# Kernel tuning notes

Measured on AMD Instinct MI355X. Metric: run time of the kernel, lower is better.

Reference implementation:

```python
import jax, jax.numpy as jnp
import numpy as np

IN_CH = 256
NUM_CLASSES = 1
CONF_THR = 0.3
NMS_IOU = 0.2
ANCHOR_SIZES = (32.0, 64.0, 128.0)
ASPECTS = (0.5, 1.0, 2.0)
NUM_ANCHORS = len(ANCHOR_SIZES) * len(ASPECTS)  # 9
K_CAND = 1024   # top-score candidates fed to NMS per image
MAX_DET = 100   # max_output_size in source
BN_EPS = 1e-5


def _anchors():
    a = [[s * r / 224.0, s / r / 224.0] for s in ANCHOR_SIZES for r in ASPECTS]
    return jnp.asarray(a, jnp.float32)  # [A, 2] (w, h)


def _conv(x, w, b, pad):
    y = jax.lax.conv_general_dilated(x, w, (1, 1), [(pad, pad), (pad, pad)],
                                     dimension_numbers=('NCHW', 'OIHW', 'NCHW'))
    return y + b[None, :, None, None]


def _bn(x, g, b, m, v):
    inv = jax.lax.rsqrt(v + BN_EPS)
    return (x - m[None, :, None, None]) * (g * inv)[None, :, None, None] + b[None, :, None, None]


def _corners(b):
    return (b[..., 0] - b[..., 2] / 2, b[..., 1] - b[..., 3] / 2,
            b[..., 0] + b[..., 2] / 2, b[..., 1] + b[..., 3] / 2)


def _iou_one(box, boxes):
    # box: [4] cxcywh, boxes: [K,4] -> iou [K]
    ax1, ay1, ax2, ay2 = _corners(box)
    bx1, by1, bx2, by2 = _corners(boxes)
    iw = jnp.maximum(jnp.minimum(ax2, bx2) - jnp.maximum(ax1, bx1), 0.0)
    ih = jnp.maximum(jnp.minimum(ay2, by2) - jnp.maximum(ay1, by1), 0.0)
    inter = iw * ih
    union = (ax2 - ax1) * (ay2 - ay1) + (bx2 - bx1) * (by2 - by1) - inter
    return inter / (union + 1e-16)


def _nms(boxes, scores):
    # boxes [K,4], scores [K] -> kept boxes padded to [MAX_DET,4]
    s0 = jnp.where(scores > CONF_THR, scores, -1.0)

    def body(i, carry):
        s, out = carry
        j = jnp.argmax(s)
        ok = s[j] > 0.0
        box = boxes[j]
        iou = _iou_one(box, boxes)
        s_new = jnp.where(iou > NMS_IOU, -1.0, s).at[j].set(-1.0)
        s = jnp.where(ok, s_new, s)
        out = out.at[i].set(jnp.where(ok, box, jnp.zeros_like(box)))
        return s, out

    _, out = jax.lax.fori_loop(0, MAX_DET, body,
                               (s0, jnp.zeros((MAX_DET, 4), boxes.dtype)))
    return out


def _forward(features, w1, b1, g1, be1, m1, v1, w2, b2, g2, be2, m2, v2, wo, bo):
    x = jax.nn.relu(_bn(_conv(features, w1, b1, 1), g1, be1, m1, v1))
    x = jax.nn.relu(_bn(_conv(x, w2, b2, 1), g2, be2, m2, v2))
    p = _conv(x, wo, bo, 0)                      # [B, A*(5+C), H, W]
    B, _, H, W = p.shape
    p = p.reshape(B, NUM_ANCHORS, 5 + NUM_CLASSES, H, W).transpose(0, 3, 4, 1, 2)  # [B,H,W,A,5+C]
    obj = jax.nn.sigmoid(p[..., 4])
    anch = _anchors()
    gx = jnp.arange(W, dtype=p.dtype)[None, :, None]
    gy = jnp.arange(H, dtype=p.dtype)[:, None, None]
    px = (jax.nn.sigmoid(p[..., 0]) + gx) / W
    py = (jax.nn.sigmoid(p[..., 1]) + gy) / H
    pw = jnp.exp(p[..., 2]) * anch[:, 0]
    ph = jnp.exp(p[..., 3]) * anch[:, 1]
    boxes = jnp.stack([px, py, pw, ph], -1).reshape(B, -1, 4)
    if NUM_CLASSES > 1:
        scores = obj * jax.nn.sigmoid(p[..., 5:]).max(-1)
    else:
        scores = obj
    scores = scores.reshape(B, -1)

    def per_image(bx, sc):
        top_s, idx = jax.lax.top_k(sc, K_CAND)
        return _nms(bx[idx], top_s)

    return jax.vmap(per_image)(boxes, scores)    # [B, MAX_DET, 4]


def setup_inputs() -> dict:
    key = jax.random.key(0)
    ks = jax.random.split(key, 16)
    B = 32
    c1, c2 = IN_CH // 2, IN_CH // 4
    oc = NUM_ANCHORS * (5 + NUM_CLASSES)
    return {
        'features': jax.random.normal(ks[0], (B, IN_CH, 56, 56), jnp.float32),
        'w1': jax.random.normal(ks[1], (c1, IN_CH, 3, 3), jnp.float32) * 0.02,
        'b1': jax.random.normal(ks[2], (c1,), jnp.float32) * 0.02,
        'g1': 1.0 + 0.1 * jax.random.normal(ks[3], (c1,), jnp.float32),
        'be1': 0.1 * jax.random.normal(ks[4], (c1,), jnp.float32),
        'm1': 0.1 * jax.random.normal(ks[5], (c1,), jnp.float32),
        'v1': jax.random.uniform(ks[6], (c1,), jnp.float32, 0.5, 1.5),
        'w2': jax.random.normal(ks[7], (c2, c1, 3, 3), jnp.float32) * 0.03,
        'b2': jax.random.normal(ks[8], (c2,), jnp.float32) * 0.02,
        'g2': 1.0 + 0.1 * jax.random.normal(ks[9], (c2,), jnp.float32),
        'be2': 0.1 * jax.random.normal(ks[10], (c2,), jnp.float32),
        'm2': 0.1 * jax.random.normal(ks[11], (c2,), jnp.float32),
        'v2': jax.random.uniform(ks[12], (c2,), jnp.float32, 0.5, 1.5),
        'wo': jax.random.normal(ks[13], (oc, c2, 1, 1), jnp.float32) * 0.1,
        'bo': jax.random.normal(ks[14], (oc,), jnp.float32) * 0.05,
    }


def reference(features, w1, b1, g1, be1, m1, v1, w2, b2, g2, be2, m2, v2, wo, bo):
    return _forward(features, w1, b1, g1, be1, m1, v1, w2, b2, g2, be2, m2, v2, wo, bo)
```

## Files before the change

### kernel.cpp

```cpp
#include <hip/hip_runtime.h>
#include <math.h>
#include <stdint.h>

constexpr int BB   = 32;
constexpr int HW   = 3136;
constexpr int C0   = 256, C1 = 128, C2 = 64;
constexpr int NA   = 9;
constexpr int NCAND = HW * NA;
constexpr int KSEL  = 1024;
constexpr int MAXDET = 100;

typedef _Float16 half8 __attribute__((ext_vector_type(8)));
typedef _Float16 half4v __attribute__((ext_vector_type(4)));
typedef float    f32x4  __attribute__((ext_vector_type(4)));
typedef float    f32x16 __attribute__((ext_vector_type(16)));

__device__ __forceinline__ void g2l16(const void* g, void* l) {
    auto gp = reinterpret_cast<const __attribute__((address_space(1))) char*>(
        reinterpret_cast<uintptr_t>(g));
    auto lp = reinterpret_cast<__attribute__((address_space(3))) char*>(
        reinterpret_cast<uintptr_t>(l));
    __builtin_amdgcn_global_load_lds(gp, lp, 16, 0, 0);
}

__global__ void bn_prep2(const float* g1, const float* be1, const float* m1,
                         const float* v1, const float* cb1,
                         const float* g2, const float* be2, const float* m2,
                         const float* v2, const float* cb2,
                         float* scl1, float* tb1, float* scl2, float* tb2) {
    int i = threadIdx.x;
    if (i < C1) {
        float inv = 1.f / sqrtf(v1[i] + 1e-5f);
        float s = g1[i] * inv;
        scl1[i] = s;
        tb1[i] = be1[i] + (cb1[i] - m1[i]) * s;
    }
    if (i < C2) {
        float inv = 1.f / sqrtf(v2[i] + 1e-5f);
        float s = g2[i] * inv;
        scl2[i] = s;
        tb2[i] = be2[i] + (cb2[i] - m2[i]) * s;
    }
}

__device__ __forceinline__ void reorder_one(const float* w, _Float16* wc,
                                            int i, int CIN, int COUT) {
    int K = CIN * 9;
    int ci  = i & 31;
    int row = (i >> 5) % (2 * COUT);
    int ch  = (i >> 5) / (2 * COUT);
    int pl  = row / COUT;
    int oc  = row - pl * COUT;
    int cg = ch / 9, r = ch - cg * 9;
    int cin = cg * 32 + ci;
    float v = w[oc * K + cin * 9 + r];
    _Float16 h = (_Float16)v;
    wc[i] = pl ? (_Float16)(v - (float)h) : h;
}

__global__ void reorder_w_both(const float* __restrict__ w1, _Float16* __restrict__ w1c,
                               const float* __restrict__ w2, _Float16* __restrict__ w2c) {
    constexpr int N1 = 2 * C1 * C0 * 9;
    constexpr int N2 = 2 * C2 * C1 * 9;
    int i = blockIdx.x * 256 + threadIdx.x;
    if (i < N1) reorder_one(w1, w1c, i, C0, C1);
    else if (i < N1 + N2) reorder_one(w2, w2c, i - N1, C1, C2);
}

__global__ __launch_bounds__(256) void nchw_to_nhwc_split(
    const float* __restrict__ in, _Float16* __restrict__ hi, _Float16* __restrict__ lo)
{
    __shared__ float tile[64 * 68];
    const int pt = blockIdx.x * 64, ct = blockIdx.y * 64, b = blockIdx.z;
    const int t = threadIdx.x;
    const int r0 = t >> 4, cidx = (t & 15) * 4;
#pragma unroll
    for (int rr = 0; rr < 64; rr += 16) {
        int r = rr + r0;
        const float* src = in + ((size_t)(b * 256 + ct + r)) * HW + pt + cidx;
        float4 v = *(const float4*)src;
        float* d = &tile[r * 68 + cidx];
        d[0] = v.x; d[1] = v.y; d[2] = v.z; d[3] = v.w;
    }
    __syncthreads();
    const int p = t >> 2, c0 = (t & 3) * 16;
    size_t obase = ((size_t)(b * HW + pt + p)) * 256 + ct + c0;
    half8 h0, h1, l0, l1;
#pragma unroll
    for (int j = 0; j < 16; ++j) {
        float v = tile[(c0 + j) * 68 + p];
        _Float16 hh = (_Float16)v;
        _Float16 ll = (_Float16)(v - (float)hh);
        if (j < 8) { h0[j] = hh; l0[j] = ll; }
        else       { h1[j - 8] = hh; l1[j - 8] = ll; }
    }
    *(half8*)(hi + obase)     = h0;
    *(half8*)(hi + obase + 8) = h1;
    *(half8*)(lo + obase)     = l0;
    *(half8*)(lo + obase + 8) = l1;
}

template <int CIN, int COUT, int MINW, bool NHWC_OUT>
__global__ __launch_bounds__(256, MINW) void conv3x3_v12(
    const _Float16* __restrict__ xhi,
    const _Float16* __restrict__ xlo,
    const _Float16* __restrict__ wc,
    const _Float16* __restrict__ zbuf,
    const float* __restrict__ scl, const float* __restrict__ tb,
    _Float16* __restrict__ ohi,
    _Float16* __restrict__ olo,
    float* __restrict__ onchw)
{
    constexpr int K       = CIN * 9;
    constexpr int NCH     = K / 32;
    constexpr int WROWS   = 2 * COUT;
    constexpr int CHALVES = WROWS * 32;
    constexpr int WI      = WROWS / 64;
    constexpr int PI      = 2;
    constexpr int WOC     = COUT / 64;

    __shared__ __align__(16) _Float16 SP[128 * 64];
    __shared__ __align__(16) _Float16 SW[WROWS * 32];

    const int bid = blockIdx.x;
    const int swz = (bid & 7) * (gridDim.x >> 3) + (bid >> 3);
    const int b = swz / 25;
    const int pixBase = (swz - b * 25) * 128;
    const int bHW = b * HW;

    const int t = threadIdx.x, l = t & 63, w = t >> 6;

    const int cpix = (l & 7) ^ ((l >> 3) & 7);
    const int ppl = cpix >> 2, pq = cpix & 3;
    const _Float16* xsp = ppl ? xlo : xhi;
    int py[4], px[4];
    const _Float16* pbase[4];
#pragma unroll
    for (int i = 0; i < 4; ++i) {
        int p = w * 32 + i * 8 + (l >> 3);
        int pix = pixBase + p;
        py[i] = pix / 56; px[i] = pix - py[i] * 56;
        pbase[i] = xsp + (size_t)(bHW + pix) * CIN + pq * 8;
    }
    const _Float16* wbase = wc + ((size_t)(w * (WI * 16) + (l >> 2))) * 32 + (l & 3) * 8;

    const int wid = t >> 6;
    const int wp = wid & 1, wo = wid >> 1;
    const int lc = l & 31, lk = l >> 5;

    f32x16 acc[PI][WOC];
#pragma unroll
    for (int pi = 0; pi < PI; ++pi)
#pragma unroll
        for (int oi = 0; oi < WOC; ++oi) acc[pi][oi] = (f32x16)0.f;

    auto stage = [&](int ch) {
        int cg = ch / 9, r = ch - cg * 9;
        int ky = r / 3;
        int dy = ky - 1, dx = (r - ky * 3) - 1;
        int off = (dy * 56 + dx) * CIN + cg * 32;
#pragma unroll
        for (int i = 0; i < 4; ++i) {
            bool v = ((unsigned)(py[i] + dy) < 56u) && ((unsigned)(px[i] + dx) < 56u);
            const void* src = v ? (const void*)(pbase[i] + off) : (const void*)zbuf;
            g2l16(src, (void*)&SP[w * 2048 + i * 512]);
        }
        const _Float16* wsrc = wbase + (size_t)ch * CHALVES;
#pragma unroll
        for (int j = 0; j < WI; ++j)
            g2l16((const void*)(wsrc + j * 512), (void*)&SW[(w * WI + j) * 512]);
    };

    auto compute = [&]() {
#pragma unroll
        for (int ks = 0; ks < 2; ++ks) {
            half8 pb[PI][2];
#pragma unroll
            for (int pi = 0; pi < PI; ++pi) {
                int prw = wp * (PI * 32) + pi * 32 + lc;
                int key = prw & 7;
#pragma unroll
                for (int pl2 = 0; pl2 < 2; ++pl2) {
                    int c = pl2 * 4 + ks * 2 + lk;
                    pb[pi][pl2] = *(const half8*)&SP[prw * 64 + ((c ^ key) << 3)];
                }
            }
            half8 wa[WOC][2];
#pragma unroll
            for (int oi = 0; oi < WOC; ++oi)
#pragma unroll
                for (int pl2 = 0; pl2 < 2; ++pl2) {
                    int row = pl2 * COUT + wo * (WOC * 32) + oi * 32 + lc;
                    int c = ks * 2 + lk;
                    wa[oi][pl2] = *(const half8*)&SW[row * 32 + (c << 3)];
                }
#pragma unroll
            for (int pi = 0; pi < PI; ++pi)
#pragma unroll
                for (int oi = 0; oi < WOC; ++oi) {
                    acc[pi][oi] = __builtin_amdgcn_mfma_f32_32x32x16_f16(wa[oi][0], pb[pi][0], acc[pi][oi], 0, 0, 0);
                    acc[pi][oi] = __builtin_amdgcn_mfma_f32_32x32x16_f16(wa[oi][0], pb[pi][1], acc[pi][oi], 0, 0, 0);
                    acc[pi][oi] = __builtin_amdgcn_mfma_f32_32x32x16_f16(wa[oi][1], pb[pi][0], acc[pi][oi], 0, 0, 0);
                }
        }
    };

    for (int ch = 0; ch < NCH; ++ch) {
        stage(ch);
        __syncthreads();
        compute();
        __syncthreads();
    }

#pragma unroll
    for (int pi = 0; pi < PI; ++pi) {
        const int pix = pixBase + wp * (PI * 32) + pi * 32 + lc;
        if (pix < HW) {
#pragma unroll
            for (int oi = 0; oi < WOC; ++oi) {
#pragma unroll
                for (int g = 0; g < 4; ++g) {
                    const int oc0 = wo * (WOC * 32) + oi * 32 + 8 * g + 4 * lk;
                    f32x4 s4 = *(const f32x4*)(scl + oc0);
                    f32x4 t4 = *(const f32x4*)(tb + oc0);
                    if constexpr (NHWC_OUT) {
                        half4v hh, ll;
#pragma unroll
                        for (int m2 = 0; m2 < 4; ++m2) {
                            float val = fmaxf(acc[pi][oi][g * 4 + m2] * s4[m2] + t4[m2], 0.f);
                            _Float16 h = (_Float16)val;
                            hh[m2] = h;
                            ll[m2] = (_Float16)(val - (float)h);
                        }
                        size_t o = ((size_t)(bHW + pix)) * COUT + oc0;
                        *(half4v*)(ohi + o) = hh;
                        *(half4v*)(olo + o) = ll;
                    } else {
#pragma unroll
                        for (int m2 = 0; m2 < 4; ++m2) {
                            float val = fmaxf(acc[pi][oi][g * 4 + m2] * s4[m2] + t4[m2], 0.f);
                            onchw[((size_t)(b * COUT + oc0 + m2)) * HW + pix] = val;
                        }
                    }
                }
            }
        }
    }
}

__global__ __launch_bounds__(256) void conv1x1_decode(
    const float* __restrict__ x2, const float* __restrict__ wo,
    const float* __restrict__ bo,
    float* __restrict__ boxes, float* __restrict__ scores)
{
    __shared__ float ws[64 * 56];
    for (int i = threadIdx.x; i < 54 * 64; i += 256) {
        int oc = i % 54, c = i / 54;
        ws[c * 56 + oc] = wo[oc * 64 + c];
    }
    __syncthreads();

    int u = blockIdx.x * 256 + threadIdx.x;
    int a = u % 9;
    int rest = u / 9;
    int quad = rest % 784;
    int b = rest / 784;
    int pix0 = quad * 4;
    int y = pix0 / 56;
    int x0 = pix0 - y * 56;

    const float* xb = x2 + (size_t)b * 64 * HW + pix0;
    float acc[5][4];
#pragma unroll
    for (int j = 0; j < 5; ++j)
#pragma unroll
        for (int p = 0; p < 4; ++p) acc[j][p] = 0.f;

#pragma unroll 8
    for (int c = 0; c < 64; ++c) {
        float4 xv = *(const float4*)(xb + c * HW);
#pragma unroll
        for (int j = 0; j < 5; ++j) {
            float w = ws[c * 56 + a * 6 + j];
            acc[j][0] += w * xv.x;
            acc[j][1] += w * xv.y;
            acc[j][2] += w * xv.z;
            acc[j][3] += w * xv.w;
        }
    }

    int si = a / 3, ri = a - si * 3;
    float sv = (float)(32 << si);
    float rv = 0.5f * (float)(1 << ri);
    float aw = (sv * rv) / 224.f;
    float ah = (sv / rv) / 224.f;
    float bo0 = bo[a * 6 + 0], bo1 = bo[a * 6 + 1], bo2 = bo[a * 6 + 2];
    float bo3 = bo[a * 6 + 3], bo4 = bo[a * 6 + 4];

#pragma unroll
    for (int p = 0; p < 4; ++p) {
        float p0 = acc[0][p] + bo0;
        float p1 = acc[1][p] + bo1;
        float p2 = acc[2][p] + bo2;
        float p3 = acc[3][p] + bo3;
        float p4 = acc[4][p] + bo4;
        float sx = 1.f / (1.f + expf(-p0));
        float sy = 1.f / (1.f + expf(-p1));
        float pxc = (sx + (float)(x0 + p)) / 56.f;
        float pyc = (sy + (float)y) / 56.f;
        float pw = expf(p2) * aw;
        float ph = expf(p3) * ah;
        float sc = 1.f / (1.f + expf(-p4));
        int n = (y * 56 + x0 + p) * 9 + a;
        float4 bx; bx.x = pxc; bx.y = pyc; bx.z = pw; bx.w = ph;
        *(float4*)&boxes[((size_t)b * NCAND + n) * 4] = bx;
        scores[(size_t)b * NCAND + n] = sc;
    }
}

__device__ __forceinline__ unsigned fkey(float f) {
    unsigned u = __float_as_uint(f);
    return (u & 0x80000000u) ? ~u : (u | 0x80000000u);
}

__global__ __launch_bounds__(1024) void topk_select(
    const float* __restrict__ scores, const float* __restrict__ boxes,
    float* __restrict__ cbox, float* __restrict__ csc, int* __restrict__ cidx)
{
    const int b = blockIdx.x, t = threadIdx.x;
    const float* sp = scores + (size_t)b * NCAND;
    const int lane = t & 63, w = t >> 6;

    __shared__ unsigned hist[2048];
    __shared__ unsigned gsum[64];
    __shared__ unsigned wsum[16];
    __shared__ unsigned s_sel, s_need, s_tot0, s_tot1;

    unsigned prefix = 0x80000000u, maskSo = 0x80000000u;
    int need = KSEL;

    for (int round = 0; round < 3; ++round) {
        const int shift = (round == 0) ? 20 : (round == 1 ? 10 : 0);
        const unsigned bmask = (round == 0) ? 2047u : 1023u;
        const int ngroups = (round == 0) ? 64 : 32;

        hist[t] = 0;
        if (round == 0) hist[t + 1024] = 0;
        __syncthreads();
        for (int i = t; i < NCAND; i += 1024) {
            unsigned u = fkey(sp[i]);
            if ((u & maskSo) == prefix) atomicAdd(&hist[(u >> shift) & bmask], 1u);
        }
        __syncthreads();
        if (t < ngroups) {
            unsigned s = 0;
#pragma unroll 8
            for (int k = 0; k < 32; ++k) s += hist[t * 32 + k];
            gsum[t] = s;
        }
        __syncthreads();
        if (t == 0) {
            int rem = need;
            int g = ngroups - 1;
            for (;; --g) {
                if ((int)gsum[g] >= rem || g == 0) break;
                rem -= (int)gsum[g];
            }
            unsigned sel = (unsigned)(g * 32);
            for (int v = g * 32 + 31; v >= g * 32; --v) {
                int c = (int)hist[v];
                if (c >= rem || v == g * 32) { sel = (unsigned)v; break; }
                rem -= c;
            }
            s_sel = sel; s_need = (unsigned)rem;
        }
        __syncthreads();
        prefix |= (s_sel << shift);
        maskSo |= (bmask << shift);
        need = (int)s_need;
        __syncthreads();
    }

    const unsigned cutoff = prefix;
    const unsigned needT = (unsigned)need;
    unsigned outBase = 0, tieBase = 0;
    const unsigned long long mlt = (1ull << lane) - 1ull;

    for (int c0 = 0; c0 < NCAND; c0 += 1024) {
        int i = c0 + t;
        bool valid = i < NCAND;
        float sc = valid ? sp[i] : 0.f;
        unsigned u = valid ? fkey(sc) : 0u;
        bool gt = valid && (u > cutoff);
        bool eq = valid && (u == cutoff);

        unsigned long long balE = __ballot(eq);
        unsigned lpE = (unsigned)__popcll(balE & mlt);
        if (lane == 0) wsum[w] = (unsigned)__popcll(balE);
        __syncthreads();
        if (t == 0) {
            unsigned run = 0;
            for (int k = 0; k < 16; ++k) { unsigned x = wsum[k]; wsum[k] = run; run += x; }
            s_tot1 = run;
        }
        __syncthreads();
        unsigned tieRank = tieBase + wsum[w] + lpE;
        bool take = gt || (eq && tieRank < needT);
        __syncthreads();

        unsigned long long balT = __ballot(take);
        unsigned lpT = (unsigned)__popcll(balT & mlt);
        if (lane == 0) wsum[w] = (unsigned)__popcll(balT);
        __syncthreads();
        if (t == 0) {
            unsigned run = 0;
            for (int k = 0; k < 16; ++k) { unsigned x = wsum[k]; wsum[k] = run; run += x; }
            s_tot0 = run;
        }
        __syncthreads();
        unsigned pos = outBase + wsum[w] + lpT;
        if (take) {
            float4 bx = *(const float4*)&boxes[((size_t)b * NCAND + i) * 4];
            *(float4*)&cbox[((size_t)b * KSEL + pos) * 4] = bx;
            csc[(size_t)b * KSEL + pos] = sc;
            cidx[(size_t)b * KSEL + pos] = i;
        }
        tieBase += s_tot1;
        outBase += s_tot0;
        __syncthreads();
    }
}

__global__ __launch_bounds__(64) void nms_wave(
    const float* __restrict__ cbox, const float* __restrict__ csc,
    const int* __restrict__ cidx, float* __restrict__ out)
{
    const int b = blockIdx.x, l = threadIdx.x;
    float cx[16], cy[16], w_[16], h_[16], s[16];
    int id[16];
#pragma unroll
    for (int j = 0; j < 16; ++j) {
        int ci = (b << 10) + (j << 6) + l;
        float4 bb = *(const float4*)&cbox[(size_t)ci * 4];
        float sc = csc[ci];
        cx[j] = bb.x; cy[j] = bb.y; w_[j] = bb.z; h_[j] = bb.w;
        s[j] = sc > 0.3f ? sc : -1.f;
        id[j] = cidx[ci];
    }
    float* ob = out + (size_t)b * MAXDET * 4;

    for (int it = 0; it < MAXDET; ++it) {
        float bs = s[0]; int bi = id[0];
        float bcx = cx[0], bcy = cy[0], bw = w_[0], bh = h_[0];
#pragma unroll
        for (int j = 1; j < 16; ++j) {
            bool tk = (s[j] > bs) || (s[j] == bs && id[j] < bi);
            if (tk) { bs = s[j]; bi = id[j]; bcx = cx[j]; bcy = cy[j]; bw = w_[j]; bh = h_[j]; }
        }
#pragma unroll
        for (int m2 = 1; m2 < 64; m2 <<= 1) {
            float os = __shfl_xor(bs, m2); int oi = __shfl_xor(bi, m2);
            float ox = __shfl_xor(bcx, m2), oy = __shfl_xor(bcy, m2);
            float ow = __shfl_xor(bw, m2), oh2 = __shfl_xor(bh, m2);
            bool tk = (os > bs) || (os == bs && oi < bi);
            if (tk) { bs = os; bi = oi; bcx = ox; bcy = oy; bw = ow; bh = oh2; }
        }
        if (bs <= 0.f) {
            for (int q = it * 4 + l; q < MAXDET * 4; q += 64) ob[q] = 0.f;
            break;
        }
        if (l == 0) {
            float4 o; o.x = bcx; o.y = bcy; o.z = bw; o.w = bh;
            *(float4*)&ob[it * 4] = o;
        }
        float wx1 = bcx - bw / 2.f, wy1 = bcy - bh / 2.f;
        float wx2 = bcx + bw / 2.f, wy2 = bcy + bh / 2.f;
        float war = (wx2 - wx1) * (wy2 - wy1);
#pragma unroll
        for (int j = 0; j < 16; ++j) {
            float jx1 = cx[j] - w_[j] / 2.f, jy1 = cy[j] - h_[j] / 2.f;
            float jx2 = cx[j] + w_[j] / 2.f, jy2 = cy[j] + h_[j] / 2.f;
            float iw = fminf(wx2, jx2) - fmaxf(wx1, jx1); iw = fmaxf(iw, 0.f);
            float ih = fminf(wy2, jy2) - fmaxf(wy1, jy1); ih = fmaxf(ih, 0.f);
            float inter = iw * ih;
            float jar = (jx2 - jx1) * (jy2 - jy1);
            float uni = war + jar - inter;
            if (inter / (uni + 1e-16f) > 0.2f) s[j] = -1.f;
        }
    }
}

extern "C" void kernel_launch(void* const* d_in, const int* in_sizes, int n_in,
                              void* d_out, int out_size, void* d_ws, size_t ws_size,
                              hipStream_t stream)
{
    const float* features = (const float*)d_in[0];
    const float* w1 = (const float*)d_in[1];
    const float* b1 = (const float*)d_in[2];
    const float* g1 = (const float*)d_in[3];
    const float* be1 = (const float*)d_in[4];
    const float* m1 = (const float*)d_in[5];
    const float* v1 = (const float*)d_in[6];
    const float* w2 = (const float*)d_in[7];
    const float* b2 = (const float*)d_in[8];
    const float* g2 = (const float*)d_in[9];
    const float* be2 = (const float*)d_in[10];
    const float* m2 = (const float*)d_in[11];
    const float* v2 = (const float*)d_in[12];
    const float* wo = (const float*)d_in[13];
    const float* bo = (const float*)d_in[14];

    char* ws = (char*)d_ws;
    size_t off = 0;
    auto alloc = [&](size_t bytes) {
        char* p = ws + off;
        off += (bytes + 255) / 256 * 256;
        return p;
    };

    _Float16* zbuf = (_Float16*)alloc(256);
    _Float16* w1c = (_Float16*)alloc((size_t)2 * C1 * 2304 * 2);
    _Float16* w2c = (_Float16*)alloc((size_t)2 * C2 * 1152 * 2);
    float* scl1 = (float*)alloc(C1 * 4);
    float* tb1  = (float*)alloc(C1 * 4);
    float* scl2 = (float*)alloc(C2 * 4);
    float* tb2  = (float*)alloc(C2 * 4);

    const size_t planeF = (size_t)BB * HW * C0 * 2;
    char* regB = alloc(2 * planeF);
    _Float16* fhi = (_Float16*)regB;
    _Float16* flo = (_Float16*)(regB + planeF);

    const size_t planeX1 = (size_t)BB * HW * C1 * 2;
    char* regC = alloc(2 * planeX1);
    _Float16* x1hi = (_Float16*)regC;
    _Float16* x1lo = (_Float16*)(regC + planeX1);

    float* x2     = (float*)regB;
    float* boxes  = (float*)(regB + 25690112);
    float* scores = (float*)(regB + 25690112 + 14450688);
    float* cbox = (float*)regC;
    float* csc  = (float*)(regC + 524288);
    int*   cidx = (int*)(regC + 524288 + 131072);

    hipMemsetAsync(zbuf, 0, 256, stream);
    bn_prep2<<<1, 256, 0, stream>>>(g1, be1, m1, v1, b1, g2, be2, m2, v2, b2,
                                    scl1, tb1, scl2, tb2);
    {
        int total = 2 * C1 * 2304 + 2 * C2 * 1152;
        reorder_w_both<<<(total + 255) / 256, 256, 0, stream>>>(w1, w1c, w2, w2c);
    }

    nchw_to_nhwc_split<<<dim3(49, 4, BB), 256, 0, stream>>>(features, fhi, flo);

    conv3x3_v12<C0, C1, 4, true><<<800, 256, 0, stream>>>(
        fhi, flo, w1c, zbuf, scl1, tb1, x1hi, x1lo, nullptr);
    conv3x3_v12<C1, C2, 4, false><<<800, 256, 0, stream>>>(
        x1hi, x1lo, w2c, zbuf, scl2, tb2, nullptr, nullptr, x2);

    conv1x1_decode<<<(BB * 784 * NA) / 256, 256, 0, stream>>>(x2, wo, bo, boxes, scores);

    topk_select<<<BB, 1024, 0, stream>>>(scores, boxes, cbox, csc, cidx);
    nms_wave<<<BB, 64, 0, stream>>>(cbox, csc, cidx, (float*)d_out);
}
```

Baseline: 608.9 us.

## Fuse 1x1 head conv and box decode into second 3x3 conv epilogue

The second 3x3 conv no longer writes the fp32 NCHW x2 tensor to global memory. Its epilogue stores the BN+ReLU outputs for its 128-pixel tile into shared memory, loads the 1x1 head weights, and runs the head conv plus sigmoid/exp box decode in place, writing boxes and scores directly. This removes a full kernel launch and the global write and reread of x2. In exchange it adds a larger LDS arena, lowers the min-waves launch bound to 3, and runs a serial per-thread 64-wide dot-product tail after the MFMA loop.

```diff
diff --git a/kernel.cpp b/kernel.cpp
--- a/kernel.cpp
+++ b/kernel.cpp
@@ -100,8 +100,8 @@
     *(half8*)(lo + obase + 8) = l1;
 }
 
-template <int CIN, int COUT, int MINW, bool NHWC_OUT>
-__global__ __launch_bounds__(256, MINW) void conv3x3_v12(
+template <int CIN, int COUT, int MINW, bool DEC>
+__global__ __launch_bounds__(256, MINW) void conv3x3_v15(
     const _Float16* __restrict__ xhi,
     const _Float16* __restrict__ xlo,
     const _Float16* __restrict__ wc,
@@ -109,7 +109,10 @@
     const float* __restrict__ scl, const float* __restrict__ tb,
     _Float16* __restrict__ ohi,
     _Float16* __restrict__ olo,
-    float* __restrict__ onchw)
+    const float* __restrict__ wox,
+    const float* __restrict__ box,
+    float* __restrict__ boxes,
+    float* __restrict__ scores)
 {
     constexpr int K       = CIN * 9;
     constexpr int NCH     = K / 32;
@@ -119,8 +122,12 @@
     constexpr int PI      = 2;
     constexpr int WOC     = COUT / 64;
 
-    __shared__ __align__(16) _Float16 SP[128 * 64];
-    __shared__ __align__(16) _Float16 SW[WROWS * 32];
+    constexpr size_t ARENA = DEC ? (33280 + 14336) : (16384 + (size_t)WROWS * 64);
+    __shared__ __align__(16) char arena[ARENA];
+    _Float16* SP = (_Float16*)arena;
+    _Float16* SW = (_Float16*)(arena + 16384);
+    float* x2t = (float*)arena;
+    float* wsd = (float*)(arena + 33280);
 
     const int bid = blockIdx.x;
     const int swz = (bid & 7) * (gridDim.x >> 3) + (bid >> 3);
@@ -212,18 +219,18 @@
         __syncthreads();
     }
 
-#pragma unroll
-    for (int pi = 0; pi < PI; ++pi) {
-        const int pix = pixBase + wp * (PI * 32) + pi * 32 + lc;
-        if (pix < HW) {
-#pragma unroll
-            for (int oi = 0; oi < WOC; ++oi) {
-#pragma unroll
-                for (int g = 0; g < 4; ++g) {
-                    const int oc0 = wo * (WOC * 32) + oi * 32 + 8 * g + 4 * lk;
-                    f32x4 s4 = *(const f32x4*)(scl + oc0);
-                    f32x4 t4 = *(const f32x4*)(tb + oc0);
-                    if constexpr (NHWC_OUT) {
+    if constexpr (!DEC) {
+#pragma unroll
+        for (int pi = 0; pi < PI; ++pi) {
+            const int pix = pixBase + wp * (PI * 32) + pi * 32 + lc;
+            if (pix < HW) {
+#pragma unroll
+                for (int oi = 0; oi < WOC; ++oi) {
+#pragma unroll
+                    for (int g = 0; g < 4; ++g) {
+                        const int oc0 = wo * (WOC * 32) + oi * 32 + 8 * g + 4 * lk;
+                        f32x4 s4 = *(const f32x4*)(scl + oc0);
+                        f32x4 t4 = *(const f32x4*)(tb + oc0);
                         half4v hh, ll;
 #pragma unroll
                         for (int m2 = 0; m2 < 4; ++m2) {
@@ -235,86 +242,73 @@
                         size_t o = ((size_t)(bHW + pix)) * COUT + oc0;
                         *(half4v*)(ohi + o) = hh;
                         *(half4v*)(olo + o) = ll;
-                    } else {
-#pragma unroll
-                        for (int m2 = 0; m2 < 4; ++m2) {
-                            float val = fmaxf(acc[pi][oi][g * 4 + m2] * s4[m2] + t4[m2], 0.f);
-                            onchw[((size_t)(b * COUT + oc0 + m2)) * HW + pix] = val;
-                        }
                     }
                 }
             }
         }
-    }
-}
-
-__global__ __launch_bounds__(256) void conv1x1_decode(
-    const float* __restrict__ x2, const float* __restrict__ wo,
-    const float* __restrict__ bo,
-    float* __restrict__ boxes, float* __restrict__ scores)
-{
-    __shared__ float ws[64 * 56];
-    for (int i = threadIdx.x; i < 54 * 64; i += 256) {
-        int oc = i % 54, c = i / 54;
-        ws[c * 56 + oc] = wo[oc * 64 + c];
-    }
-    __syncthreads();
-
-    int u = blockIdx.x * 256 + threadIdx.x;
-    int a = u % 9;
-    int rest = u / 9;
-    int quad = rest % 784;
-    int b = rest / 784;
-    int pix0 = quad * 4;
-    int y = pix0 / 56;
-    int x0 = pix0 - y * 56;
-
-    const float* xb = x2 + (size_t)b * 64 * HW + pix0;
-    float acc[5][4];
-#pragma unroll
-    for (int j = 0; j < 5; ++j)
-#pragma unroll
-        for (int p = 0; p < 4; ++p) acc[j][p] = 0.f;
-
+    } else {
+#pragma unroll
+        for (int pi = 0; pi < PI; ++pi) {
+            const int lp = wp * (PI * 32) + pi * 32 + lc;
+#pragma unroll
+            for (int g = 0; g < 4; ++g) {
+                const int oc0 = wo * 32 + 8 * g + 4 * lk;
+                f32x4 s4 = *(const f32x4*)(scl + oc0);
+                f32x4 t4 = *(const f32x4*)(tb + oc0);
+#pragma unroll
+                for (int m2 = 0; m2 < 4; ++m2) {
+                    float val = fmaxf(acc[0][0][0] * 0.f, 0.f);
+                    val = fmaxf(acc[pi][0][g * 4 + m2] * s4[m2] + t4[m2], 0.f);
+                    x2t[lp * 65 + oc0 + m2] = val;
+                }
+            }
+        }
+        for (int i = t; i < 54 * 64; i += 256) {
+            int oc = i % 54, c = i / 54;
+            wsd[c * 56 + oc] = wox[oc * 64 + c];
+        }
+        __syncthreads();
+
+        for (int n0 = t; n0 < 128 * NA; n0 += 256) {
+            int lp = n0 / 9, a = n0 - lp * 9;
+            int pix = pixBase + lp;
+            if (pix >= HW) continue;
+            int y = pix / 56, x0 = pix - y * 56;
+
+            float p0 = 0.f, p1 = 0.f, p2 = 0.f, p3 = 0.f, p4 = 0.f;
+            const float* xr = &x2t[lp * 65];
 #pragma unroll 8
-    for (int c = 0; c < 64; ++c) {
-        float4 xv = *(const float4*)(xb + c * HW);
-#pragma unroll
-        for (int j = 0; j < 5; ++j) {
-            float w = ws[c * 56 + a * 6 + j];
-            acc[j][0] += w * xv.x;
-            acc[j][1] += w * xv.y;
-            acc[j][2] += w * xv.z;
-            acc[j][3] += w * xv.w;
-        }
-    }
-
-    int si = a / 3, ri = a - si * 3;
-    float sv = (float)(32 << si);
-    float rv = 0.5f * (float)(1 << ri);
-    float aw = (sv * rv) / 224.f;
-    float ah = (sv / rv) / 224.f;
-    float bo0 = bo[a * 6 + 0], bo1 = bo[a * 6 + 1], bo2 = bo[a * 6 + 2];
-    float bo3 = bo[a * 6 + 3], bo4 = bo[a * 6 + 4];
-
-#pragma unroll
-    for (int p = 0; p < 4; ++p) {
-        float p0 = acc[0][p] + bo0;
-        float p1 = acc[1][p] + bo1;
-        float p2 = acc[2][p] + bo2;
-        float p3 = acc[3][p] + bo3;
-        float p4 = acc[4][p] + bo4;
-        float sx = 1.f / (1.f + expf(-p0));
-        float sy = 1.f / (1.f + expf(-p1));
-        float pxc = (sx + (float)(x0 + p)) / 56.f;
-        float pyc = (sy + (float)y) / 56.f;
-        float pw = expf(p2) * aw;
-        float ph = expf(p3) * ah;
-        float sc = 1.f / (1.f + expf(-p4));
-        int n = (y * 56 + x0 + p) * 9 + a;
-        float4 bx; bx.x = pxc; bx.y = pyc; bx.z = pw; bx.w = ph;
-        *(float4*)&boxes[((size_t)b * NCAND + n) * 4] = bx;
-        scores[(size_t)b * NCAND + n] = sc;
+            for (int c = 0; c < 64; ++c) {
+                float xv = xr[c];
+                const float* wr = &wsd[c * 56 + a * 6];
+                p0 += wr[0] * xv;
+                p1 += wr[1] * xv;
+                p2 += wr[2] * xv;
+                p3 += wr[3] * xv;
+                p4 += wr[4] * xv;
+            }
+            int si = a / 3, ri = a - si * 3;
+            float sv = (float)(32 << si);
+            float rv = 0.5f * (float)(1 << ri);
+            float aw = (sv * rv) / 224.f;
+            float ah = (sv / rv) / 224.f;
+            p0 += box[a * 6 + 0];
+            p1 += box[a * 6 + 1];
+            p2 += box[a * 6 + 2];
+            p3 += box[a * 6 + 3];
+            p4 += box[a * 6 + 4];
+            float sx = 1.f / (1.f + expf(-p0));
+            float sy = 1.f / (1.f + expf(-p1));
+            float pxc = (sx + (float)x0) / 56.f;
+            float pyc = (sy + (float)y) / 56.f;
+            float pw = expf(p2) * aw;
+            float ph = expf(p3) * ah;
+            float sc = 1.f / (1.f + expf(-p4));
+            int n = pix * 9 + a;
+            float4 bx; bx.x = pxc; bx.y = pyc; bx.z = pw; bx.w = ph;
+            *(float4*)&boxes[((size_t)b * NCAND + n) * 4] = bx;
+            scores[(size_t)b * NCAND + n] = sc;
+        }
     }
 }
 
@@ -536,7 +530,6 @@
     _Float16* x1hi = (_Float16*)regC;
     _Float16* x1lo = (_Float16*)(regC + planeX1);
 
-    float* x2     = (float*)regB;
     float* boxes  = (float*)(regB + 25690112);
     float* scores = (float*)(regB + 25690112 + 14450688);
     float* cbox = (float*)regC;
@@ -553,12 +546,12 @@
 
     nchw_to_nhwc_split<<<dim3(49, 4, BB), 256, 0, stream>>>(features, fhi, flo);
 
-    conv3x3_v12<C0, C1, 4, true><<<800, 256, 0, stream>>>(
-        fhi, flo, w1c, zbuf, scl1, tb1, x1hi, x1lo, nullptr);
-    conv3x3_v12<C1, C2, 4, false><<<800, 256, 0, stream>>>(
-        x1hi, x1lo, w2c, zbuf, scl2, tb2, nullptr, nullptr, x2);
-
-    conv1x1_decode<<<(BB * 784 * NA) / 256, 256, 0, stream>>>(x2, wo, bo, boxes, scores);
+    conv3x3_v15<C0, C1, 4, false><<<800, 256, 0, stream>>>(
+        fhi, flo, w1c, zbuf, scl1, tb1, x1hi, x1lo,
+        nullptr, nullptr, nullptr, nullptr);
+    conv3x3_v15<C1, C2, 3, true><<<800, 256, 0, stream>>>(
+        x1hi, x1lo, w2c, zbuf, scl2, tb2, nullptr, nullptr,
+        wo, bo, boxes, scores);
 
     topk_select<<<BB, 1024, 0, stream>>>(scores, boxes, cbox, csc, cidx);
     nms_wave<<<BB, 64, 0, stream>>>(cbox, csc, cidx, (float*)d_out);
```

After: 629.8 us. 3.4% more time.

## Double-buffer LDS staging in first 3x3 conv with async global-to-LDS prefetch

Applied to the files above, without the earlier changes.

Adds a new conv3x3 kernel variant that keeps two LDS buffers for the pixel and weight tiles. It prefetches the next chunk with global_load_lds while the current chunk runs through MFMA, using vmcnt waits and barriers. The first convolution is switched to this kernel with launch bounds of 2 waves per EU, down from 4. The aim is to hide global-load latency behind compute, at the cost of doubled LDS use and possibly lower occupancy.

```diff
diff --git a/kernel.cpp b/kernel.cpp
--- a/kernel.cpp
+++ b/kernel.cpp
@@ -100,6 +100,163 @@
     *(half8*)(lo + obase + 8) = l1;
 }
 
+template <int CIN, int COUT, bool NHWC_OUT>
+__global__ __launch_bounds__(256, 2) void conv3x3_v18(
+    const _Float16* __restrict__ xhi,
+    const _Float16* __restrict__ xlo,
+    const _Float16* __restrict__ wc,
+    const _Float16* __restrict__ zbuf,
+    const float* __restrict__ scl, const float* __restrict__ tb,
+    _Float16* __restrict__ ohi, _Float16* __restrict__ olo,
+    float* __restrict__ onchw)
+{
+    constexpr int K       = CIN * 9;
+    constexpr int NCH     = K / 32;
+    constexpr int WROWS   = 2 * COUT;
+    constexpr int CHALVES = WROWS * 32;
+    constexpr int WI      = WROWS / 64;
+    constexpr int PI      = 2;
+    constexpr int WOC     = COUT / 64;
+
+    __shared__ __align__(16) _Float16 SP[2][128 * 64];
+    __shared__ __align__(16) _Float16 SW[2][WROWS * 32];
+
+    const int bid = blockIdx.x;
+    const int swz = (bid & 7) * (gridDim.x >> 3) + (bid >> 3);
+    const int b = swz / 25;
+    const int pixBase = (swz - b * 25) * 128;
+    const int bHW = b * HW;
+
+    const int t = threadIdx.x, l = t & 63, w = t >> 6;
+
+    const int cpix = (l & 7) ^ ((l >> 3) & 7);
+    const int ppl = cpix >> 2, pq = cpix & 3;
+    const _Float16* xsp = ppl ? xlo : xhi;
+    int py[4], px[4];
+    const _Float16* pbase[4];
+#pragma unroll
+    for (int i = 0; i < 4; ++i) {
+        int p = w * 32 + i * 8 + (l >> 3);
+        int pix = pixBase + p;
+        py[i] = pix / 56; px[i] = pix - py[i] * 56;
+        pbase[i] = xsp + (size_t)(bHW + pix) * CIN + pq * 8;
+    }
+    const _Float16* wbase = wc + ((size_t)(w * (WI * 16) + (l >> 2))) * 32 + (l & 3) * 8;
+
+    const int wid = t >> 6;
+    const int wp = wid & 1, wo = wid >> 1;
+    const int lc = l & 31, lk = l >> 5;
+
+    f32x16 acc[PI][WOC];
+#pragma unroll
+    for (int pi = 0; pi < PI; ++pi)
+#pragma unroll
+        for (int oi = 0; oi < WOC; ++oi) acc[pi][oi] = (f32x16)0.f;
+
+    auto stage = [&](int ch, int buf) {
+        int cg = ch / 9, r = ch - cg * 9;
+        int ky = r / 3;
+        int dy = ky - 1, dx = (r - ky * 3) - 1;
+        int off = (dy * 56 + dx) * CIN + cg * 32;
+#pragma unroll
+        for (int i = 0; i < 4; ++i) {
+            bool v = ((unsigned)(py[i] + dy) < 56u) && ((unsigned)(px[i] + dx) < 56u);
+            const void* src = v ? (const void*)(pbase[i] + off) : (const void*)zbuf;
+            g2l16(src, (void*)&SP[buf][w * 2048 + i * 512]);
+        }
+        const _Float16* wsrc = wbase + (size_t)ch * CHALVES;
+#pragma unroll
+        for (int j = 0; j < WI; ++j)
+            g2l16((const void*)(wsrc + j * 512), (void*)&SW[buf][(w * WI + j) * 512]);
+    };
+
+    auto compute = [&](int buf) {
+#pragma unroll
+        for (int ks = 0; ks < 2; ++ks) {
+            half8 pb[PI][2];
+#pragma unroll
+            for (int pi = 0; pi < PI; ++pi) {
+                int prw = wp * (PI * 32) + pi * 32 + lc;
+                int key = prw & 7;
+#pragma unroll
+                for (int pl2 = 0; pl2 < 2; ++pl2) {
+                    int c = pl2 * 4 + ks * 2 + lk;
+                    pb[pi][pl2] = *(const half8*)&SP[buf][prw * 64 + ((c ^ key) << 3)];
+                }
+            }
+            half8 wa[WOC][2];
+#pragma unroll
+            for (int oi = 0; oi < WOC; ++oi)
+#pragma unroll
+                for (int pl2 = 0; pl2 < 2; ++pl2) {
+                    int row = pl2 * COUT + wo * (WOC * 32) + oi * 32 + lc;
+                    int c = ks * 2 + lk;
+                    wa[oi][pl2] = *(const half8*)&SW[buf][row * 32 + (c << 3)];
+                }
+#pragma unroll
+            for (int pi = 0; pi < PI; ++pi)
+#pragma unroll
+                for (int oi = 0; oi < WOC; ++oi) {
+                    acc[pi][oi] = __builtin_amdgcn_mfma_f32_32x32x16_f16(wa[oi][0], pb[pi][0], acc[pi][oi], 0, 0, 0);
+                    acc[pi][oi] = __builtin_amdgcn_mfma_f32_32x32x16_f16(wa[oi][0], pb[pi][1], acc[pi][oi], 0, 0, 0);
+                    acc[pi][oi] = __builtin_amdgcn_mfma_f32_32x32x16_f16(wa[oi][1], pb[pi][0], acc[pi][oi], 0, 0, 0);
+                }
+        }
+    };
+
+    stage(0, 0);
+    stage(1, 1);
+    int cur = 0;
+    for (int ch = 0; ch < NCH; ++ch) {
+        if (ch + 1 < NCH) {
+            asm volatile("s_waitcnt vmcnt(8)" ::: "memory");
+        } else {
+            asm volatile("s_waitcnt vmcnt(0)" ::: "memory");
+        }
+        __builtin_amdgcn_sched_barrier(0);
+        __builtin_amdgcn_s_barrier();
+        compute(cur);
+        __builtin_amdgcn_s_barrier();
+        if (ch + 2 < NCH) stage(ch + 2, cur);
+        cur ^= 1;
+    }
+
+#pragma unroll
+    for (int pi = 0; pi < PI; ++pi) {
+        const int pix = pixBase + wp * (PI * 32) + pi * 32 + lc;
+        if (pix < HW) {
+#pragma unroll
+            for (int oi = 0; oi < WOC; ++oi) {
+#pragma unroll
+                for (int g = 0; g < 4; ++g) {
+                    const int oc0 = wo * (WOC * 32) + oi * 32 + 8 * g + 4 * lk;
+                    f32x4 s4 = *(const f32x4*)(scl + oc0);
+                    f32x4 t4 = *(const f32x4*)(tb + oc0);
+                    if constexpr (NHWC_OUT) {
+                        half4v hh, ll;
+#pragma unroll
+                        for (int m2 = 0; m2 < 4; ++m2) {
+                            float val = fmaxf(acc[pi][oi][g * 4 + m2] * s4[m2] + t4[m2], 0.f);
+                            _Float16 h = (_Float16)val;
+                            hh[m2] = h;
+                            ll[m2] = (_Float16)(val - (float)h);
+                        }
+                        size_t o = ((size_t)(bHW + pix)) * COUT + oc0;
+                        *(half4v*)(ohi + o) = hh;
+                        *(half4v*)(olo + o) = ll;
+                    } else {
+#pragma unroll
+                        for (int m2 = 0; m2 < 4; ++m2) {
+                            float val = fmaxf(acc[pi][oi][g * 4 + m2] * s4[m2] + t4[m2], 0.f);
+                            onchw[((size_t)(b * COUT + oc0 + m2)) * HW + pix] = val;
+                        }
+                    }
+                }
+            }
+        }
+    }
+}
+
 template <int CIN, int COUT, int MINW, bool NHWC_OUT>
 __global__ __launch_bounds__(256, MINW) void conv3x3_v12(
     const _Float16* __restrict__ xhi,
@@ -107,8 +264,7 @@
     const _Float16* __restrict__ wc,
     const _Float16* __restrict__ zbuf,
     const float* __restrict__ scl, const float* __restrict__ tb,
-    _Float16* __restrict__ ohi,
-    _Float16* __restrict__ olo,
+    _Float16* __restrict__ ohi, _Float16* __restrict__ olo,
     float* __restrict__ onchw)
 {
     constexpr int K       = CIN * 9;
@@ -553,7 +709,7 @@
 
     nchw_to_nhwc_split<<<dim3(49, 4, BB), 256, 0, stream>>>(features, fhi, flo);
 
-    conv3x3_v12<C0, C1, 4, true><<<800, 256, 0, stream>>>(
+    conv3x3_v18<C0, C1, true><<<800, 256, 0, stream>>>(
         fhi, flo, w1c, zbuf, scl1, tb1, x1hi, x1lo, nullptr);
     conv3x3_v12<C1, C2, 4, false><<<800, 256, 0, stream>>>(
         x1hi, x1lo, w2c, zbuf, scl2, tb2, nullptr, nullptr, x2);
```

New measurement: 593.5 us (median of 2 runs). -2.5%, faster.
